# Kernel tuning notes

Hardware: AMD Instinct MI355X
Metric: run time of the kernel (lower is better)

The kernel has to match this reference:

```python
import jax, jax.numpy as jnp
import numpy as np

B, N, S, F = 16384, 1152, 576, 8  # batch, n_sites, n_symm, features
LOG2 = float(np.log(2.0))


def log_cosh(x):
    # numerically stable log(cosh(x)) = |x| + log1p(exp(-2|x|)) - log(2)
    a = jnp.abs(x)
    return a + jnp.log1p(jnp.exp(-2.0 * a)) - LOG2


def setup_inputs() -> dict:
    key = jax.random.key(0)
    ks = iter(jax.random.split(key, 32))
    f32 = jnp.float32
    d = {}
    d['x'] = jax.random.normal(next(ks), (B, N), dtype=f32)
    d['symmetries'] = jax.random.randint(next(ks), (S, N), 0, N, dtype=jnp.int32)
    d['corr0'] = jax.random.randint(next(ks), (576, 4), 0, N, dtype=jnp.int32)
    d['corr1'] = jax.random.randint(next(ks), (576, 4), 0, N, dtype=jnp.int32)
    d['corr2'] = jax.random.randint(next(ks), (24, 24), 0, N, dtype=jnp.int32)
    d['corr3'] = jax.random.randint(next(ks), (24, 24), 0, N, dtype=jnp.int32)
    d['corr0_symm'] = jax.random.randint(next(ks), (S, 576), 0, 576, dtype=jnp.int32)
    d['corr1_symm'] = jax.random.randint(next(ks), (S, 576), 0, 576, dtype=jnp.int32)
    d['corr2_symm'] = jax.random.randint(next(ks), (S, 24), 0, 24, dtype=jnp.int32)
    d['corr3_symm'] = jax.random.randint(next(ks), (S, 24), 0, 24, dtype=jnp.int32)
    std = 0.01
    d['hidden_bias'] = std * jax.random.normal(next(ks), (F,), dtype=f32)
    d['symm_kernel'] = std * jax.random.normal(next(ks), (F, N), dtype=f32)
    d['visible_bias'] = std * jax.random.normal(next(ks), (2,), dtype=f32)
    d['corr0_bias'] = std * jax.random.normal(next(ks), (1,), dtype=f32)
    d['corr0_kernel'] = std * jax.random.normal(next(ks), (F, 576), dtype=f32)
    d['corr1_bias'] = std * jax.random.normal(next(ks), (1,), dtype=f32)
    d['corr1_kernel'] = std * jax.random.normal(next(ks), (F, 576), dtype=f32)
    d['corr2_bias'] = std * jax.random.normal(next(ks), (1,), dtype=f32)
    d['corr2_kernel'] = std * jax.random.normal(next(ks), (F, 24), dtype=f32)
    d['corr3_bias'] = std * jax.random.normal(next(ks), (1,), dtype=f32)
    d['corr3_kernel'] = std * jax.random.normal(next(ks), (F, 24), dtype=f32)
    d['loop0_hidden_bias'] = std * jax.random.normal(next(ks), (F,), dtype=f32)
    d['loop0_kernel'] = std * jax.random.normal(next(ks), (F, 24), dtype=f32)
    d['loop1_hidden_bias'] = std * jax.random.normal(next(ks), (F,), dtype=f32)
    d['loop1_kernel'] = std * jax.random.normal(next(ks), (F, 24), dtype=f32)
    return d


def reference(x, symmetries, corr0, corr1, corr2, corr3,
              corr0_symm, corr1_symm, corr2_symm, corr3_symm,
              hidden_bias, symm_kernel, visible_bias,
              corr0_bias, corr0_kernel, corr1_bias, corr1_kernel,
              corr2_bias, corr2_kernel, corr3_bias, corr3_kernel,
              loop0_hidden_bias, loop0_kernel, loop1_hidden_bias, loop1_kernel):
    n_batch = x.shape[0]
    # symmetrized kernel: (F, S, N)
    K = jnp.take(symm_kernel, symmetries, axis=1)
    theta = jnp.einsum('bn,fsn->bfs', x, K)  # (B, F, S)
    theta = theta + hidden_bias[:, None]
    bias = jnp.sum(x.reshape(n_batch, -1, 2), axis=1) @ visible_bias  # (B,)

    correlators = [corr0, corr1, corr2, corr3]
    corr_symms = [corr0_symm, corr1_symm, corr2_symm, corr3_symm]
    corr_biases = [corr0_bias, corr1_bias, corr2_bias, corr3_bias]
    corr_kernels = [corr0_kernel, corr1_kernel, corr2_kernel, corr3_kernel]

    corr_values = []
    for corr, csym, cb, ck in zip(correlators, corr_symms, corr_biases, corr_kernels):
        ckk = jnp.take(ck, csym, axis=1)               # (F, S, C)
        cv = jnp.take(x, corr, axis=1).prod(axis=2)    # (B, C)
        corr_values.append(cv)
        theta = theta + jnp.einsum('bc,fsc->bfs', cv, ckk)
        bias = bias + cb * jnp.sum(cv, axis=1)

    out = jnp.sum(log_cosh(theta), axis=(1, 2))  # (B,)

    # last two correlators are loop correlators with dedicated hidden units
    loop_params = [(loop0_hidden_bias, loop0_kernel, corr2_symm, corr_values[2]),
                   (loop1_hidden_bias, loop1_kernel, corr3_symm, corr_values[3])]
    for lhb, lk, lsym, lv in loop_params:
        lkk = jnp.take(lk, lsym, axis=1)                      # (F, S, C)
        lt = jnp.einsum('bc,fsc->bfs', lv, lkk) + lhb[:, None]
        out = out + jnp.sum(log_cosh(lt), axis=(1, 2))

    return out + bias
```

## Files before the change

### kernel.cpp

```cpp
#include <hip/hip_runtime.h>
#include <math.h>

#define B_    16384
#define N_    1152
#define KPAD  2464
#define NK32  77
#define KLOOP 256
#define NOUT  4608
#define NT2   18
#define LOG2F_ 0.69314718055994530942f

typedef unsigned short ushort_t;
typedef __attribute__((ext_vector_type(8))) short short8;
typedef __attribute__((ext_vector_type(4))) float floatx4;

__device__ __forceinline__ float log_cosh_f(float t) {
    float a = fabsf(t);
    return a + __logf(1.0f + __expf(-2.0f * a)) - LOG2F_;
}
__device__ __forceinline__ ushort_t bf16_rne(float f) {
    unsigned int u = __float_as_uint(f);
    return (ushort_t)((u + 0x7fffu + ((u >> 16) & 1u)) >> 16);
}
__device__ __forceinline__ float bf16_to_f(ushort_t h) {
    return __uint_as_float(((unsigned int)h) << 16);
}

typedef __attribute__((address_space(1))) const unsigned int guint;
typedef __attribute__((address_space(3))) unsigned int luint;
__device__ __forceinline__ void gload16(const ushort_t* src, ushort_t* dst) {
    __builtin_amdgcn_global_load_lds((guint*)src, (luint*)dst, 16, 0, 0);
}

#define PIPE_WAIT(N) do {                                     \
    asm volatile("s_waitcnt vmcnt(" #N ")" ::: "memory");     \
    __builtin_amdgcn_s_barrier();                             \
    asm volatile("" ::: "memory"); } while (0)

__global__ __launch_bounds__(256) void build_w(
    const int* __restrict__ symm,
    const int* __restrict__ c0s, const int* __restrict__ c1s,
    const int* __restrict__ c2s, const int* __restrict__ c3s,
    const float* __restrict__ sk,
    const float* __restrict__ ck0, const float* __restrict__ ck1,
    const float* __restrict__ ck2, const float* __restrict__ ck3,
    const float* __restrict__ l0k, const float* __restrict__ l1k,
    ushort_t* __restrict__ Wb, ushort_t* __restrict__ LWb)
{
    __shared__ int idx[2352];
    const int s = blockIdx.x;
    const int tid = threadIdx.x;
    for (int i = tid; i < 1152; i += 256) idx[i] = symm[s * N_ + i];
    for (int i = tid; i < 576; i += 256) idx[1152 + i] = c0s[s * 576 + i];
    for (int i = tid; i < 576; i += 256) idx[1728 + i] = c1s[s * 576 + i];
    if (tid < 24) idx[2304 + tid] = c2s[s * 24 + tid];
    else if (tid < 48) idx[2328 + (tid - 24)] = c3s[s * 24 + (tid - 24)];
    __syncthreads();
    for (int f = 0; f < 8; ++f) {
        ushort_t* wr = Wb + (size_t)(s * 8 + f) * KPAD;
        for (int k = tid; k < KPAD; k += 256) {
            ushort_t o;
            if (k < 1152)      o = bf16_rne(sk[f * N_ + idx[k]]);
            else if (k < 1728) o = bf16_rne(ck0[f * 576 + idx[k]]);
            else if (k < 2304) o = bf16_rne(ck1[f * 576 + idx[k]]);
            else if (k < 2448) {
                int q = k - 2304, g = q / 48, c = q - g * 48;
                float w = (c < 24) ? ck2[f * 24 + idx[2304 + c]]
                                   : ck3[f * 24 + idx[2328 + (c - 24)]];
                ushort_t hi = bf16_rne(w);
                o = (g < 2) ? hi : bf16_rne(w - bf16_to_f(hi));
            } else o = 0;
            wr[k] = o;
        }
        ushort_t* lr = LWb + (size_t)(s * 8 + f) * KLOOP;
        for (int k2 = tid; k2 < KLOOP; k2 += 256) {
            int j2 = k2 >> 7, q = k2 & 127;
            ushort_t o = 0;
            if (q < 72) {
                int g = q / 24, c = q - g * 24;
                float w = j2 ? l1k[f * 24 + idx[2328 + c]]
                             : l0k[f * 24 + idx[2304 + c]];
                ushort_t hi = bf16_rne(w);
                o = (g < 2) ? hi : bf16_rne(w - bf16_to_f(hi));
            }
            lr[k2] = o;
        }
    }
}

__global__ __launch_bounds__(256) void build_cv(
    const float* __restrict__ x,
    const int* __restrict__ corr0, const int* __restrict__ corr1,
    const int* __restrict__ corr2, const int* __restrict__ corr3,
    const float* __restrict__ vb,
    const float* __restrict__ cb0, const float* __restrict__ cb1,
    const float* __restrict__ cb2, const float* __restrict__ cb3,
    ushort_t* __restrict__ XA, ushort_t* __restrict__ CVL,
    float* __restrict__ initb)
{
    __shared__ float xs[N_];
    __shared__ float red[256];
    __shared__ float cvhi[48], cvlo[48];
    const int tid = threadIdx.x;
    const int b = blockIdx.x;
    ushort_t* xr = XA + (size_t)b * KPAD;

    float bias = 0.f;
    const float vb0 = vb[0], vb1 = vb[1];
    for (int i = tid; i < N_; i += 256) {
        float v = x[(size_t)b * N_ + i];
        xs[i] = v;
        bias += v * ((i & 1) ? vb1 : vb0);
        xr[i] = bf16_rne(v);
    }
    __syncthreads();
    float s0 = 0.f, s1 = 0.f, s2 = 0.f, s3 = 0.f;
    for (int c = tid; c < 576; c += 256) {
        const int* i0 = corr0 + c * 4;
        float p = xs[i0[0]] * xs[i0[1]] * xs[i0[2]] * xs[i0[3]];
        xr[1152 + c] = bf16_rne(p); s0 += p;
        const int* i1 = corr1 + c * 4;
        float q = xs[i1[0]] * xs[i1[1]] * xs[i1[2]] * xs[i1[3]];
        xr[1728 + c] = bf16_rne(q); s1 += q;
    }
    if (tid < 48) {
        int j2 = tid / 24, c = tid - j2 * 24;
        const int* ii = (j2 ? corr3 : corr2) + c * 24;
        float p = 1.f;
        for (int j = 0; j < 24; ++j) p *= xs[ii[j]];
        float hv = bf16_to_f(bf16_rne(p));
        cvhi[tid] = hv;
        cvlo[tid] = p - hv;
        if (j2) s3 = p; else s2 = p;
    }
    __syncthreads();
    for (int i = tid; i < KPAD - 2304; i += 256) {
        ushort_t o = 0;
        if (i < 144) {
            int g = i / 48, c = i - g * 48;
            o = bf16_rne(g == 1 ? cvlo[c] : cvhi[c]);
        }
        xr[2304 + i] = o;
    }
    ushort_t* cr = CVL + (size_t)b * KLOOP;
    for (int k2 = tid; k2 < KLOOP; k2 += 256) {
        int j2 = k2 >> 7, q = k2 & 127;
        ushort_t o = 0;
        if (q < 72) {
            int g = q / 24, c = q - g * 24;
            o = bf16_rne(g == 1 ? cvlo[j2 * 24 + c] : cvhi[j2 * 24 + c]);
        }
        cr[k2] = o;
    }
    bias += cb0[0] * s0 + cb1[0] * s1 + cb2[0] * s2 + cb3[0] * s3;
    red[tid] = bias;
    __syncthreads();
    for (int off = 128; off; off >>= 1) {
        if (tid < off) red[tid] += red[tid + off];
        __syncthreads();
    }
    if (tid == 0) initb[b] = red[0];
}

__global__ __launch_bounds__(512, 2) void mfma_gemm(
    const ushort_t* __restrict__ XA, const ushort_t* __restrict__ Wb,
    const ushort_t* __restrict__ CVL, const ushort_t* __restrict__ LWb,
    const float* __restrict__ hidden_bias,
    const float* __restrict__ l0hb, const float* __restrict__ l1hb,
    float* __restrict__ partials)
{
    __shared__ __align__(16) ushort_t sh[65536];
    ushort_t* const A0 = sh;                 ushort_t* const Bu0 = sh + 8192;
    ushort_t* const A1 = sh + 16384;         ushort_t* const Bu1 = sh + 24576;
    ushort_t* const A2 = sh + 32768;         ushort_t* const Bu2 = sh + 40960;
    ushort_t* const A3 = sh + 49152;         ushort_t* const Bu3 = sh + 57344;

    const int tid = threadIdx.x;
    const int l = tid & 63, w = tid >> 6;
    const int wm = w >> 2, wn = w & 3;
    const int lrow = l & 15, lg = l >> 4;
    const int srow = l >> 2;
    const int sgr8 = ((l & 3) ^ ((srow >> 1) & 3)) * 8;

    const int bid = blockIdx.x;
    const int swz = (bid & 7) * 144 + (bid >> 3);
    const int nt = swz % NT2, bt = swz / NT2;
    const int n0 = nt * 256, b0 = bt * 256;

    const ushort_t* XAb  = XA  + (size_t)b0 * KPAD;
    const ushort_t* Wbb  = Wb  + (size_t)n0 * KPAD;
    const ushort_t* CVb  = CVL + (size_t)b0 * KLOOP;
    const ushort_t* LWbb = LWb + (size_t)n0 * KLOOP;

    floatx4 acc[8][4];

    auto STG = [&](const ushort_t* g, int stride, int kg, ushort_t* lbase) {
#pragma unroll
        for (int i = 0; i < 2; ++i) {
            const int r0 = i * 128 + w * 16;
            gload16(g + (size_t)(r0 + srow) * stride + kg + sgr8,
                    lbase + r0 * 32);
        }
    };

    const int ga = (lg ^ ((lrow >> 1) & 3)) * 8;
    const int abase = (wm * 128 + lrow) * 32 + ga;
    const int bbase = (wn * 64 + lrow) * 32 + ga;

    auto TILE2 = [&](const ushort_t* Ab, const ushort_t* Bb,
                     int kgn, ushort_t* An, ushort_t* Bn, bool doStage) {
        short8 af[4], af2[4], bfr[4];
#pragma unroll
        for (int mi = 0; mi < 4; ++mi)
            af[mi] = *(const short8*)(Ab + abase + mi * 512);
#pragma unroll
        for (int ni = 0; ni < 4; ++ni)
            bfr[ni] = *(const short8*)(Bb + bbase + ni * 512);
        if (doStage) STG(XAb, KPAD, kgn, An);
        __builtin_amdgcn_sched_barrier(0);
        __builtin_amdgcn_s_barrier();
        asm volatile("s_waitcnt lgkmcnt(0)" ::: "memory");
        __builtin_amdgcn_sched_barrier(0);
        __builtin_amdgcn_s_setprio(1);
#pragma unroll
        for (int mi = 0; mi < 4; ++mi)
#pragma unroll
            for (int ni = 0; ni < 4; ++ni)
                acc[mi][ni] = __builtin_amdgcn_mfma_f32_16x16x32_bf16(
                    af[mi], bfr[ni], acc[mi][ni], 0, 0, 0);
        __builtin_amdgcn_s_setprio(0);
        __builtin_amdgcn_s_barrier();
#pragma unroll
        for (int mi = 0; mi < 4; ++mi)
            af2[mi] = *(const short8*)(Ab + abase + 2048 + mi * 512);
        if (doStage) STG(Wbb, KPAD, kgn, Bn);
        __builtin_amdgcn_sched_barrier(0);
        __builtin_amdgcn_s_barrier();
        asm volatile("s_waitcnt lgkmcnt(0)" ::: "memory");
        __builtin_amdgcn_sched_barrier(0);
        __builtin_amdgcn_s_setprio(1);
#pragma unroll
        for (int mi = 0; mi < 4; ++mi)
#pragma unroll
            for (int ni = 0; ni < 4; ++ni)
                acc[mi + 4][ni] = __builtin_amdgcn_mfma_f32_16x16x32_bf16(
                    af2[mi], bfr[ni], acc[mi + 4][ni], 0, 0, 0);
        __builtin_amdgcn_s_setprio(0);
        __builtin_amdgcn_s_barrier();
    };

#pragma unroll
    for (int mi = 0; mi < 8; ++mi)
#pragma unroll
        for (int ni = 0; ni < 4; ++ni) acc[mi][ni] = (floatx4){0.f, 0.f, 0.f, 0.f};

    STG(XAb, KPAD, 0, A0);  STG(Wbb, KPAD, 0, Bu0);
    STG(XAb, KPAD, 32, A1); STG(Wbb, KPAD, 32, Bu1);
    STG(XAb, KPAD, 64, A2); STG(Wbb, KPAD, 64, Bu2);
#pragma unroll 1
    for (int tt = 0; tt < 18; ++tt) {
        const int t = tt * 4;
        PIPE_WAIT(8); TILE2(A0, Bu0, (t + 3) * 32, A3, Bu3, true);
        PIPE_WAIT(8); TILE2(A1, Bu1, (t + 4) * 32, A0, Bu0, true);
        PIPE_WAIT(8); TILE2(A2, Bu2, (t + 5) * 32, A1, Bu1, true);
        PIPE_WAIT(8); TILE2(A3, Bu3, (t + 6) * 32, A2, Bu2, true);
    }
    PIPE_WAIT(8); TILE2(A0, Bu0, 75 * 32, A3, Bu3, true);
    PIPE_WAIT(8); TILE2(A1, Bu1, 76 * 32, A0, Bu0, true);
    PIPE_WAIT(8); TILE2(A2, Bu2, 0, A1, Bu1, false);
    PIPE_WAIT(4); TILE2(A3, Bu3, 0, A1, Bu1, false);
    PIPE_WAIT(0); TILE2(A0, Bu0, 0, A1, Bu1, false);

    float rs[32];
    {
        const float hbv = hidden_bias[l & 7];
#pragma unroll
        for (int mi = 0; mi < 8; ++mi)
#pragma unroll
            for (int reg = 0; reg < 4; ++reg) {
                float t = 0.f;
#pragma unroll
                for (int ni = 0; ni < 4; ++ni)
                    t += log_cosh_f(acc[mi][ni][reg] + hbv);
                rs[mi * 4 + reg] = t;
            }
    }

#pragma unroll 1
    for (int j2 = 0; j2 < 2; ++j2) {
#pragma unroll
        for (int mi = 0; mi < 8; ++mi)
#pragma unroll
            for (int ni = 0; ni < 4; ++ni) acc[mi][ni] = (floatx4){0.f, 0.f, 0.f, 0.f};
        __syncthreads();
        STG(CVb, KLOOP, j2 * 128 +  0, A0); STG(LWbb, KLOOP, j2 * 128 +  0, Bu0);
        STG(CVb, KLOOP, j2 * 128 + 32, A1); STG(LWbb, KLOOP, j2 * 128 + 32, Bu1);
        STG(CVb, KLOOP, j2 * 128 + 64, A2); STG(LWbb, KLOOP, j2 * 128 + 64, Bu2);
        STG(CVb, KLOOP, j2 * 128 + 96, A3); STG(LWbb, KLOOP, j2 * 128 + 96, Bu3);
        __syncthreads();
        TILE2(A0, Bu0, 0, A1, Bu1, false);
        TILE2(A1, Bu1, 0, A1, Bu1, false);
        TILE2(A2, Bu2, 0, A1, Bu1, false);
        TILE2(A3, Bu3, 0, A1, Bu1, false);
        const float lbv = (j2 ? l1hb : l0hb)[l & 7];
#pragma unroll
        for (int mi = 0; mi < 8; ++mi)
#pragma unroll
            for (int reg = 0; reg < 4; ++reg) {
                float t = 0.f;
#pragma unroll
                for (int ni = 0; ni < 4; ++ni)
                    t += log_cosh_f(acc[mi][ni][reg] + lbv);
                rs[mi * 4 + reg] += t;
            }
    }

    __syncthreads();
    float* red = (float*)sh;
#pragma unroll
    for (int mi = 0; mi < 8; ++mi)
#pragma unroll
        for (int reg = 0; reg < 4; ++reg) {
            float v = rs[mi * 4 + reg];
            v += __shfl_xor(v, 1);
            v += __shfl_xor(v, 2);
            v += __shfl_xor(v, 4);
            v += __shfl_xor(v, 8);
            if (lrow == 0)
                red[(wm * 128 + mi * 16 + lg * 4 + reg) * 5 + wn] = v;
        }
    __syncthreads();
    if (tid < 256) {
        float t = red[tid * 5 + 0] + red[tid * 5 + 1] +
                  red[tid * 5 + 2] + red[tid * 5 + 3];
        partials[(size_t)nt * B_ + b0 + tid] = t;
    }
}

__global__ __launch_bounds__(256) void finalize_out(
    const float* __restrict__ initb, const float* __restrict__ partials,
    float* __restrict__ out)
{
    int b = blockIdx.x * 256 + threadIdx.x;
    float s = initb[b];
#pragma unroll
    for (int t = 0; t < NT2; ++t) s += partials[(size_t)t * B_ + b];
    out[b] = s;
}

extern "C" void kernel_launch(void* const* d_in, const int* in_sizes, int n_in,
                              void* d_out, int out_size, void* d_ws, size_t ws_size,
                              hipStream_t stream) {
    const float* x    = (const float*)d_in[0];
    const int* symm   = (const int*)d_in[1];
    const int* corr0  = (const int*)d_in[2];
    const int* corr1  = (const int*)d_in[3];
    const int* corr2  = (const int*)d_in[4];
    const int* corr3  = (const int*)d_in[5];
    const int* c0s    = (const int*)d_in[6];
    const int* c1s    = (const int*)d_in[7];
    const int* c2s    = (const int*)d_in[8];
    const int* c3s    = (const int*)d_in[9];
    const float* hb   = (const float*)d_in[10];
    const float* sk   = (const float*)d_in[11];
    const float* vb   = (const float*)d_in[12];
    const float* cb0  = (const float*)d_in[13];
    const float* ck0  = (const float*)d_in[14];
    const float* cb1  = (const float*)d_in[15];
    const float* ck1  = (const float*)d_in[16];
    const float* cb2  = (const float*)d_in[17];
    const float* ck2  = (const float*)d_in[18];
    const float* cb3  = (const float*)d_in[19];
    const float* ck3  = (const float*)d_in[20];
    const float* l0hb = (const float*)d_in[21];
    const float* l0k  = (const float*)d_in[22];
    const float* l1hb = (const float*)d_in[23];
    const float* l1k  = (const float*)d_in[24];

    ushort_t* wsu = (ushort_t*)d_ws;
    ushort_t* Wb  = wsu;
    ushort_t* XA  = Wb + (size_t)NOUT * KPAD;
    ushort_t* LWb = XA + (size_t)B_ * KPAD;
    ushort_t* CVL = LWb + (size_t)NOUT * KLOOP;
    float* initb    = (float*)(CVL + (size_t)B_ * KLOOP);
    float* partials = initb + B_;

    build_w<<<576, 256, 0, stream>>>(
        symm, c0s, c1s, c2s, c3s, sk, ck0, ck1, ck2, ck3, l0k, l1k, Wb, LWb);
    build_cv<<<B_, 256, 0, stream>>>(
        x, corr0, corr1, corr2, corr3, vb, cb0, cb1, cb2, cb3, XA, CVL, initb);
    mfma_gemm<<<1152, 512, 0, stream>>>(
        XA, Wb, CVL, LWb, hb, l0hb, l1hb, partials);
    finalize_out<<<B_ / 256, 256, 0, stream>>>(initb, partials, (float*)d_out);
}
```

Before: 613.2 us.

## Restructure GEMM main loop into double-buffered 64-wide K stages with per-phase waits

New measurement: 610.9 us. Within noise of the previous version (-0.4%).

```diff
diff --git a/kernel.cpp b/kernel.cpp
--- a/kernel.cpp
+++ b/kernel.cpp
@@ -3,8 +3,8 @@
 
 #define B_    16384
 #define N_    1152
-#define KPAD  2464
-#define NK32  77
+#define KPAD  2496
+#define NKT   39
 #define KLOOP 256
 #define NOUT  4608
 #define NT2   18
@@ -31,11 +31,6 @@
 __device__ __forceinline__ void gload16(const ushort_t* src, ushort_t* dst) {
     __builtin_amdgcn_global_load_lds((guint*)src, (luint*)dst, 16, 0, 0);
 }
-
-#define PIPE_WAIT(N) do {                                     \
-    asm volatile("s_waitcnt vmcnt(" #N ")" ::: "memory");     \
-    __builtin_amdgcn_s_barrier();                             \
-    asm volatile("" ::: "memory"); } while (0)
 
 __global__ __launch_bounds__(256) void build_w(
     const int* __restrict__ symm,
@@ -170,10 +165,6 @@
     float* __restrict__ partials)
 {
     __shared__ __align__(16) ushort_t sh[65536];
-    ushort_t* const A0 = sh;                 ushort_t* const Bu0 = sh + 8192;
-    ushort_t* const A1 = sh + 16384;         ushort_t* const Bu1 = sh + 24576;
-    ushort_t* const A2 = sh + 32768;         ushort_t* const Bu2 = sh + 40960;
-    ushort_t* const A3 = sh + 49152;         ushort_t* const Bu3 = sh + 57344;
 
     const int tid = threadIdx.x;
     const int l = tid & 63, w = tid >> 6;
@@ -193,13 +184,14 @@
     const ushort_t* LWbb = LWb + (size_t)n0 * KLOOP;
 
     floatx4 acc[8][4];
-
-    auto STG = [&](const ushort_t* g, int stride, int kg, ushort_t* lbase) {
+    short8 bfr[4];
+
+    auto STG = [&](const ushort_t* g, int stride, int kg, int ldsOff) {
 #pragma unroll
         for (int i = 0; i < 2; ++i) {
             const int r0 = i * 128 + w * 16;
             gload16(g + (size_t)(r0 + srow) * stride + kg + sgr8,
-                    lbase + r0 * 32);
+                    &sh[ldsOff + r0 * 32]);
         }
     };
 
@@ -207,16 +199,19 @@
     const int abase = (wm * 128 + lrow) * 32 + ga;
     const int bbase = (wn * 64 + lrow) * 32 + ga;
 
-    auto TILE2 = [&](const ushort_t* Ab, const ushort_t* Bb,
-                     int kgn, ushort_t* An, ushort_t* Bn, bool doStage) {
-        short8 af[4], af2[4], bfr[4];
+    auto PHASE = [&](int asrc, int bsrc, int mih,
+                     const ushort_t* sg, int sstride, int skg, int sdst,
+                     int vf) {
+        short8 afb[4];
+        if (mih == 0) {
+#pragma unroll
+            for (int ni = 0; ni < 4; ++ni)
+                bfr[ni] = *(const short8*)&sh[bsrc + bbase + ni * 512];
+        }
 #pragma unroll
         for (int mi = 0; mi < 4; ++mi)
-            af[mi] = *(const short8*)(Ab + abase + mi * 512);
-#pragma unroll
-        for (int ni = 0; ni < 4; ++ni)
-            bfr[ni] = *(const short8*)(Bb + bbase + ni * 512);
-        if (doStage) STG(XAb, KPAD, kgn, An);
+            afb[mi] = *(const short8*)&sh[asrc + abase + mih * 2048 + mi * 512];
+        if (sg) STG(sg, sstride, skg, sdst);
         __builtin_amdgcn_sched_barrier(0);
         __builtin_amdgcn_s_barrier();
         asm volatile("s_waitcnt lgkmcnt(0)" ::: "memory");
@@ -226,27 +221,13 @@
         for (int mi = 0; mi < 4; ++mi)
 #pragma unroll
             for (int ni = 0; ni < 4; ++ni)
-                acc[mi][ni] = __builtin_amdgcn_mfma_f32_16x16x32_bf16(
-                    af[mi], bfr[ni], acc[mi][ni], 0, 0, 0);
+                acc[mih * 4 + mi][ni] = __builtin_amdgcn_mfma_f32_16x16x32_bf16(
+                    afb[mi], bfr[ni], acc[mih * 4 + mi][ni], 0, 0, 0);
         __builtin_amdgcn_s_setprio(0);
-        __builtin_amdgcn_s_barrier();
-#pragma unroll
-        for (int mi = 0; mi < 4; ++mi)
-            af2[mi] = *(const short8*)(Ab + abase + 2048 + mi * 512);
-        if (doStage) STG(Wbb, KPAD, kgn, Bn);
+        if (vf == 1) asm volatile("s_waitcnt vmcnt(4)" ::: "memory");
+        else if (vf == 2) asm volatile("s_waitcnt vmcnt(0)" ::: "memory");
         __builtin_amdgcn_sched_barrier(0);
         __builtin_amdgcn_s_barrier();
-        asm volatile("s_waitcnt lgkmcnt(0)" ::: "memory");
-        __builtin_amdgcn_sched_barrier(0);
-        __builtin_amdgcn_s_setprio(1);
-#pragma unroll
-        for (int mi = 0; mi < 4; ++mi)
-#pragma unroll
-            for (int ni = 0; ni < 4; ++ni)
-                acc[mi + 4][ni] = __builtin_amdgcn_mfma_f32_16x16x32_bf16(
-                    af2[mi], bfr[ni], acc[mi + 4][ni], 0, 0, 0);
-        __builtin_amdgcn_s_setprio(0);
-        __builtin_amdgcn_s_barrier();
     };
 
 #pragma unroll
@@ -254,22 +235,26 @@
 #pragma unroll
         for (int ni = 0; ni < 4; ++ni) acc[mi][ni] = (floatx4){0.f, 0.f, 0.f, 0.f};
 
-    STG(XAb, KPAD, 0, A0);  STG(Wbb, KPAD, 0, Bu0);
-    STG(XAb, KPAD, 32, A1); STG(Wbb, KPAD, 32, Bu1);
-    STG(XAb, KPAD, 64, A2); STG(Wbb, KPAD, 64, Bu2);
+    STG(XAb, KPAD, 0, 0);      STG(Wbb, KPAD, 0, 8192);
+    STG(XAb, KPAD, 32, 16384); STG(Wbb, KPAD, 32, 24576);
+    asm volatile("s_waitcnt vmcnt(4)" ::: "memory");
+    __builtin_amdgcn_s_barrier();
+
 #pragma unroll 1
-    for (int tt = 0; tt < 18; ++tt) {
-        const int t = tt * 4;
-        PIPE_WAIT(8); TILE2(A0, Bu0, (t + 3) * 32, A3, Bu3, true);
-        PIPE_WAIT(8); TILE2(A1, Bu1, (t + 4) * 32, A0, Bu0, true);
-        PIPE_WAIT(8); TILE2(A2, Bu2, (t + 5) * 32, A1, Bu1, true);
-        PIPE_WAIT(8); TILE2(A3, Bu3, (t + 6) * 32, A2, Bu2, true);
-    }
-    PIPE_WAIT(8); TILE2(A0, Bu0, 75 * 32, A3, Bu3, true);
-    PIPE_WAIT(8); TILE2(A1, Bu1, 76 * 32, A0, Bu0, true);
-    PIPE_WAIT(8); TILE2(A2, Bu2, 0, A1, Bu1, false);
-    PIPE_WAIT(4); TILE2(A3, Bu3, 0, A1, Bu1, false);
-    PIPE_WAIT(0); TILE2(A0, Bu0, 0, A1, Bu1, false);
+    for (int t = 0; t < NKT - 1; ++t) {
+        const int cb = (t & 1) * 32768, nb = cb ^ 32768;
+        const int kg = (t + 1) * 64;
+        PHASE(cb,         cb + 8192,  0, XAb, KPAD, kg,      nb,         0);
+        PHASE(cb,         cb + 8192,  1, Wbb, KPAD, kg,      nb + 8192,  1);
+        PHASE(cb + 16384, cb + 24576, 0, XAb, KPAD, kg + 32, nb + 16384, 0);
+        PHASE(cb + 16384, cb + 24576, 1, Wbb, KPAD, kg + 32, nb + 24576, 1);
+    }
+    {
+        PHASE(0,     8192,  0, nullptr, 0, 0, 0, 0);
+        PHASE(0,     8192,  1, nullptr, 0, 0, 0, 2);
+        PHASE(16384, 24576, 0, nullptr, 0, 0, 0, 0);
+        PHASE(16384, 24576, 1, nullptr, 0, 0, 0, 0);
+    }
 
     float rs[32];
     {
@@ -293,15 +278,20 @@
 #pragma unroll
             for (int ni = 0; ni < 4; ++ni) acc[mi][ni] = (floatx4){0.f, 0.f, 0.f, 0.f};
         __syncthreads();
-        STG(CVb, KLOOP, j2 * 128 +  0, A0); STG(LWbb, KLOOP, j2 * 128 +  0, Bu0);
-        STG(CVb, KLOOP, j2 * 128 + 32, A1); STG(LWbb, KLOOP, j2 * 128 + 32, Bu1);
-        STG(CVb, KLOOP, j2 * 128 + 64, A2); STG(LWbb, KLOOP, j2 * 128 + 64, Bu2);
-        STG(CVb, KLOOP, j2 * 128 + 96, A3); STG(LWbb, KLOOP, j2 * 128 + 96, Bu3);
+        const int kb = j2 * 128;
+        STG(CVb, KLOOP, kb,      0);      STG(LWbb, KLOOP, kb,      8192);
+        STG(CVb, KLOOP, kb + 32, 16384);  STG(LWbb, KLOOP, kb + 32, 24576);
+        STG(CVb, KLOOP, kb + 64, 32768);  STG(LWbb, KLOOP, kb + 64, 40960);
+        STG(CVb, KLOOP, kb + 96, 49152);  STG(LWbb, KLOOP, kb + 96, 57344);
         __syncthreads();
-        TILE2(A0, Bu0, 0, A1, Bu1, false);
-        TILE2(A1, Bu1, 0, A1, Bu1, false);
-        TILE2(A2, Bu2, 0, A1, Bu1, false);
-        TILE2(A3, Bu3, 0, A1, Bu1, false);
+        PHASE(0,     8192,  0, nullptr, 0, 0, 0, 0);
+        PHASE(0,     8192,  1, nullptr, 0, 0, 0, 0);
+        PHASE(16384, 24576, 0, nullptr, 0, 0, 0, 0);
+        PHASE(16384, 24576, 1, nullptr, 0, 0, 0, 0);
+        PHASE(32768, 40960, 0, nullptr, 0, 0, 0, 0);
+        PHASE(32768, 40960, 1, nullptr, 0, 0, 0, 0);
+        PHASE(49152, 57344, 0, nullptr, 0, 0, 0, 0);
+        PHASE(49152, 57344, 1, nullptr, 0, 0, 0, 0);
         const float lbv = (j2 ? l1hb : l0hb)[l & 7];
 #pragma unroll
         for (int mi = 0; mi < 8; ++mi)
```
